# Kernel optimization log

Measured on AMD Instinct MI355X. Metric: run time of the kernel, lower is better.

The kernel has to match this reference:

```python
import jax, jax.numpy as jnp
import numpy as np

STATE_DIM = 1024
INPUT_DIM = 256
OUTPUT_DIM = 256
KX = 10
LAM = 5.0
BSZ = 16
SEQ = 2048


def setup_inputs() -> dict:
    key = jax.random.key(0)
    ks = jax.random.split(key, 6)
    inputs = jax.random.normal(ks[0], (BSZ, SEQ, INPUT_DIM), dtype=jnp.float32)
    h0 = jax.random.normal(ks[1], (STATE_DIM,), dtype=jnp.float32)
    # exponential_decay_init: entries in (exp(-lam), 1)
    A = jnp.exp(-LAM * jax.random.uniform(ks[2], (STATE_DIM,), dtype=jnp.float32))
    B = jax.random.normal(ks[3], (INPUT_DIM, STATE_DIM), dtype=jnp.float32) / INPUT_DIM
    C = jax.random.normal(ks[4], (STATE_DIM, OUTPUT_DIM), dtype=jnp.float32) / STATE_DIM
    M = jax.random.normal(ks[5], (OUTPUT_DIM, INPUT_DIM, KX), dtype=jnp.float32) / OUTPUT_DIM
    return {"inputs": inputs, "h0": h0, "A": A, "B": B, "C": C, "M": M}


def _lds_forward(inputs, h0, A, B, C, M):
    bsz, L, _ = inputs.shape
    S = A.shape[0]
    kx = M.shape[-1]
    # input projection: u_t @ B  -> [B, L, S]
    uB = jnp.einsum('bld,ds->bls', inputs, B)
    # diagonal linear recurrence h_t = A * h_{t-1} + uB_t, h_{-1} = h0,
    # via parallel associative scan on affine maps (a, b): h -> a*h + b
    a = jnp.broadcast_to(A, (1, L, S))

    def combine(x, y):
        a1, b1 = x
        a2, b2 = y
        return (a1 * a2, a2 * b1 + b2)

    Pa, Pb = jax.lax.associative_scan(combine, (a, uB), axis=1)
    all_h = Pa * h0 + Pb                              # [B, L, S]
    lds_out = jnp.einsum('bls,so->blo', all_h, C)      # [B, L, O]
    # shift forward by kx: new[:, :-kx] = lds_out[:, kx:], tail zeros
    new_lds = jnp.pad(lds_out[:, kx:, :], ((0, 0), (0, kx), (0, 0)))
    # AR term: ar[b,t,o] = sum_{i<kx} M[o,:,i] . x[b, t-i, :] (zero-padded past)
    ar = jnp.zeros_like(new_lds)
    for i in range(kx):
        x_i = jnp.pad(inputs, ((0, 0), (i, 0), (0, 0)))[:, :L, :]
        ar = ar + jnp.einsum('oj,blj->blo', M[:, :, i], x_i)
    return ar + new_lds


def reference(inputs, h0, A, B, C, M):
    return _lds_forward(inputs, h0, A, B, C, M)
```

## Files before the change

### kernel.cpp

```cpp
#include <hip/hip_runtime.h>

#define BSZn 16
#define SEQn 2048
#define DIN 256
#define DST 1024
#define DOUTn 256
#define KXn 10
#define TCH 64
#define NCH 32

typedef __attribute__((ext_vector_type(4))) float f32x4;
typedef __attribute__((ext_vector_type(8))) short bf16x8;

__device__ __forceinline__ unsigned short f2bf(float f){
  unsigned u = __float_as_uint(f);
  u += 0x7FFF + ((u>>16)&1);
  return (unsigned short)(u>>16);
}
__device__ __forceinline__ float bf2f(unsigned short s){
  return __uint_as_float(((unsigned)s)<<16);
}

#define XIDX(r,c) ((((r)<<8) + (c)) ^ (((r)&7)<<3))


__global__ void k_prep(const float* __restrict__ B, const float* __restrict__ C,
                       const float* __restrict__ M, unsigned short* __restrict__ Bt2,
                       unsigned short* __restrict__ Ct2, unsigned short* __restrict__ Mt2){
  int stride = gridDim.x*blockDim.x;
  int i0 = blockIdx.x*blockDim.x + threadIdx.x;
  for(int idx=i0; idx<DIN*DST; idx+=stride){
    int kb = idx>>15, s = (idx>>5)&1023, dl = idx&31;
    int d = (kb<<5)+dl;
    Bt2[idx] = f2bf(B[d*DST + s]);
  }
  for(int idx=i0; idx<DST*DOUTn; idx+=stride){
    int kb = idx>>13, o = (idx>>5)&255, sl = idx&31;
    int s = (kb<<5)+sl;
    Ct2[idx] = f2bf(C[s*DOUTn + o]);
  }
  for(int idx=i0; idx<DOUTn*DIN*KXn; idx+=stride){
    int kq = idx>>13, o = (idx>>5)&255, kl = idx&31;
    int k = (kq<<5)+kl, ii = k>>8, j = k&255;
    Mt2[idx] = f2bf(M[(o*DIN+j)*KXn + ii]);
  }
}

__global__ __launch_bounds__(256) void k_ub(const float* __restrict__ x,
    const unsigned short* __restrict__ Bt2, const float* __restrict__ A,
    unsigned short* __restrict__ uB, float* __restrict__ P){
  __shared__ __align__(16) unsigned short xt[64*256];
  int wg = blockIdx.x;
  int q = wg & 3, c = (wg>>2)&31, b = wg>>7;
  int t0 = c*TCH, s0 = q<<8;
  const float* xb = x + (size_t)b*SEQn*DIN;
  int tid = threadIdx.x;
  for(int e = tid; e < 64*64; e += 256){
    int r = e>>6, c4 = (e&63)<<2;
    float4 v = *(const float4*)(xb + (t0+r)*DIN + c4);
    ushort4 w; w.x=f2bf(v.x); w.y=f2bf(v.y); w.z=f2bf(v.z); w.w=f2bf(v.w);
    *(ushort4*)&xt[XIDX(r,c4)] = w;
  }
  __syncthreads();
  int wv = tid>>6, ln = tid&63, lm = ln&15, lk = (ln>>4)<<3, rr = (ln>>4)<<2;
  f32x4 zf = {0.f,0.f,0.f,0.f};
  f32x4 acc[4][4];
  #pragma unroll
  for(int tt=0;tt<4;tt++)
    #pragma unroll
    for(int nt=0;nt<4;nt++) acc[tt][nt] = zf;
  #pragma unroll
  for(int kb=0;kb<8;kb++){
    bf16x8 af[4];
    #pragma unroll
    for(int tt=0;tt<4;tt++)
      af[tt] = *(const bf16x8*)&xt[XIDX((tt<<4)+lm, (kb<<5)+lk)];
    #pragma unroll
    for(int nt=0;nt<4;nt++){
      int sg = s0 + (wv<<6) + (nt<<4) + lm;
      bf16x8 bfr = *(const bf16x8*)&Bt2[(kb<<15) + (sg<<5) + lk];
      #pragma unroll
      for(int tt=0;tt<4;tt++)
        acc[tt][nt] = __builtin_amdgcn_mfma_f32_16x16x32_bf16(af[tt], bfr, acc[tt][nt], 0,0,0);
    }
  }
  __syncthreads();
  #pragma unroll
  for(int tt=0;tt<4;tt++)
    #pragma unroll
    for(int nt=0;nt<4;nt++)
      #pragma unroll
      for(int r4=0;r4<4;r4++)
        xt[XIDX((tt<<4)+rr+r4, (wv<<6)+(nt<<4)+lm)] = f2bf(acc[tt][nt][r4]);
  __syncthreads();
  unsigned short* hb = uB + ((size_t)b*129)*32*512;
  #pragma unroll
  for(int it=0; it<8; it++){
    int j = it*256 + tid;
    int r = j>>5, c0 = (j&31)<<3;
    bf16x8 v = *(const bf16x8*)&xt[XIDX(r,c0)];
    int s = s0 + c0;
    size_t addr = (((size_t)(c*4 + (r>>4)))*32 + (s>>5))*512 + ((r&15)<<5) + (s&31);
    *(bf16x8*)&hb[addr] = v;
  }
  if(c == 31){
    unsigned* zp = (unsigned*)(uB + (((size_t)b*129 + 128)*32 + (q<<3))*512);
    for(int e = tid; e < 2048; e += 256) zp[e] = 0u;
  }
  {
    int s = s0 + tid;
    float Av = A[s];
    float p = 0.f;
    #pragma unroll
    for(int t=0;t<64;t++)
      p = fmaf(Av, p, bf2f(xt[XIDX(t, tid)]));
    P[(((b<<5)+c)<<10) + s] = p;
  }
}

__global__ void k_bound(const float* __restrict__ A, const float* __restrict__ h0,
                        const float* __restrict__ P, float* __restrict__ bound){
  int i = blockIdx.x*blockDim.x + threadIdx.x;
  if(i >= BSZn*DST) return;
  int b = i >> 10, s = i & 1023;
  float Av = A[s];
  float a2=Av*Av, a4=a2*a2, a8=a4*a4, a16=a8*a8, a32=a16*a16, a64=a32*a32;
  const float* Pb = P + ((size_t)(b<<5)<<10);
  float* Bb = bound + ((size_t)(b<<5)<<10);
  float h = h0[s];
  Bb[s] = h;
  for(int c=1;c<NCH;c++){
    h = fmaf(a64, h, Pb[((c-1)<<10)+s]);
    Bb[(c<<10)+s] = h;
  }
}

__global__ __launch_bounds__(256) void k_h(unsigned short* __restrict__ uB,
    const float* __restrict__ A, const float* __restrict__ bound){
  int wg = blockIdx.x;
  int half = wg & 1, c = (wg>>1) & 31, b = wg >> 6;
  int tid = threadIdx.x;
  int s = (half<<9) + (tid<<1);
  float Av0 = A[s], Av1 = A[s+1];
  const float* bp = bound + (((size_t)(b<<5)+c)<<10) + s;
  float h0v = bp[0], h1v = bp[1];
  unsigned short* hb = uB + (((size_t)b*129 + c*4)*32 + (s>>5))*512 + (s&31);
  #pragma unroll 4
  for(int t=0;t<64;t++){
    unsigned* p = (unsigned*)(hb + ((t>>4)*32*512) + ((t&15)<<5));
    unsigned v = *p;
    h0v = fmaf(Av0, h0v, bf2f((unsigned short)(v & 0xffff)));
    h1v = fmaf(Av1, h1v, bf2f((unsigned short)(v >> 16)));
    *p = (unsigned)f2bf(h0v) | (((unsigned)f2bf(h1v))<<16);
  }
}

__global__ __launch_bounds__(256,4) void k_arc(const float* __restrict__ x,
    const unsigned short* __restrict__ Mt2, const unsigned short* __restrict__ Ct2,
    const unsigned short* __restrict__ h2, float* __restrict__ out){
  __shared__ __align__(16) unsigned short xt[73*256];
  int wg = blockIdx.x;
  int oh = wg & 1, c = (wg>>1)&31, b = wg>>6;
  int t0 = c*TCH;
  const float* xb = x + (size_t)b*SEQn*DIN;
  int tid = threadIdx.x;
  for(int e = tid; e < 73*64; e += 256){
    int r = e>>6, c4 = (e&63)<<2;
    int t = t0 - 9 + r;
    float4 v = {0.f,0.f,0.f,0.f};
    if(t >= 0) v = *(const float4*)(xb + t*DIN + c4);
    ushort4 w; w.x=f2bf(v.x); w.y=f2bf(v.y); w.z=f2bf(v.z); w.w=f2bf(v.w);
    *(ushort4*)&xt[XIDX(r, c4)] = w;
  }
  __syncthreads();
  int wv = tid>>6, ln = tid&63, lm = ln&15, lk = (ln>>4)<<3, rr = (ln>>4)<<2;
  int obase = (oh<<7) + (wv<<5);
  f32x4 zf = {0.f,0.f,0.f,0.f};
  f32x4 acc[4][2];
  #pragma unroll
  for(int tt=0;tt<4;tt++)
    #pragma unroll
    for(int nt=0;nt<2;nt++) acc[tt][nt] = zf;
  for(int i=0;i<KXn;i++){
    #pragma unroll
    for(int kb8=0;kb8<8;kb8++){
      int col = (kb8<<5) + lk;
      int kq = i*8 + kb8;
      bf16x8 af[4];
      #pragma unroll
      for(int tt=0;tt<4;tt++)
        af[tt] = *(const bf16x8*)&xt[XIDX((tt<<4)+lm + 9 - i, col)];
      #pragma unroll
      for(int nt=0;nt<2;nt++){
        int o = obase + (nt<<4) + lm;
        bf16x8 bfr = *(const bf16x8*)&Mt2[(kq<<13) + (o<<5) + lk];
        #pragma unroll
        for(int tt=0;tt<4;tt++)
          acc[tt][nt] = __builtin_amdgcn_mfma_f32_16x16x32_bf16(af[tt], bfr, acc[tt][nt], 0,0,0);
      }
    }
  }
  const unsigned short* hb = h2 + (size_t)b*129*32*512;
  int Tg0 = c*4 + (lm>=6 ? 1 : 0);
  int rowin = (lm<6) ? (10+lm) : (lm-6);
  #pragma unroll
  for(int kb=0;kb<32;kb++){
    bf16x8 af[4];
    #pragma unroll
    for(int tt=0;tt<4;tt++)
      af[tt] = *(const bf16x8*)&hb[(((size_t)(Tg0+tt))*32 + kb)*512 + rowin*32 + lk];
    #pragma unroll
    for(int nt=0;nt<2;nt++){
      int o = obase + (nt<<4) + lm;
      bf16x8 bfr = *(const bf16x8*)&Ct2[(kb<<13) + (o<<5) + lk];
      #pragma unroll
      for(int tt=0;tt<4;tt++)
        acc[tt][nt] = __builtin_amdgcn_mfma_f32_16x16x32_bf16(af[tt], bfr, acc[tt][nt], 0,0,0);
    }
  }
  #pragma unroll
  for(int tt=0;tt<4;tt++)
    #pragma unroll
    for(int nt=0;nt<2;nt++)
      #pragma unroll
      for(int r4=0;r4<4;r4++){
        int m = (tt<<4) + rr + r4;
        int o = obase + (nt<<4) + lm;
        out[((size_t)b*SEQn + t0 + m)*DOUTn + o] = acc[tt][nt][r4];
      }
}

extern "C" void kernel_launch(void* const* d_in, const int* in_sizes, int n_in,
                              void* d_out, int out_size, void* d_ws, size_t ws_size,
                              hipStream_t stream){
  const float* x  = (const float*)d_in[0];
  const float* h0 = (const float*)d_in[1];
  const float* A  = (const float*)d_in[2];
  const float* B  = (const float*)d_in[3];
  const float* C  = (const float*)d_in[4];
  const float* M  = (const float*)d_in[5];
  float* out = (float*)d_out;
  unsigned short* Bt2 = (unsigned short*)d_ws;
  unsigned short* Ct2 = Bt2 + DIN*DST;
  unsigned short* Mt2 = Ct2 + DST*DOUTn;
  float* P     = (float*)((char*)d_ws + ( 4u<<20));
  float* bound = (float*)((char*)d_ws + ( 6u<<20));
  unsigned short* uB = (unsigned short*)((char*)d_ws + (8u<<20));
  k_prep <<<512, 256, 0, stream>>>(B, C, M, Bt2, Ct2, Mt2);
  k_ub   <<<BSZn*NCH*4, 256, 0, stream>>>(x, Bt2, A, uB, P);
  k_bound<<<(BSZn*DST)/256, 256, 0, stream>>>(A, h0, P, bound);
  k_h    <<<BSZn*NCH*2, 256, 0, stream>>>(uB, A, bound);
  k_arc  <<<BSZn*NCH*2, 256, 0, stream>>>(x, Mt2, Ct2, uB, out);
}
```

Before: 276.8 us.

## Fold chunk-boundary scan into k_h, coalesce prep reads, widen k_arc output tile

Three changes. The separate k_bound launch is removed: each k_h block now recomputes its chunk's starting state by serially folding the prior chunk sums P with A^64, which drops one launch and the bound buffer but adds up to 31 redundant reads per block. k_prep now reads the weights coalesced and scatters the bf16 writes. k_arc now has each block compute all 256 outputs (4x4 MFMA tiles per wave) with half the blocks, so each block loads the x tile once instead of twice, at the cost of more registers and less parallelism (launch bounds 256,2).

Result: faster. 255.8 us (-7.6%).

```diff
diff --git a/kernel.cpp b/kernel.cpp
--- a/kernel.cpp
+++ b/kernel.cpp
@@ -30,19 +30,18 @@
   int stride = gridDim.x*blockDim.x;
   int i0 = blockIdx.x*blockDim.x + threadIdx.x;
   for(int idx=i0; idx<DIN*DST; idx+=stride){
-    int kb = idx>>15, s = (idx>>5)&1023, dl = idx&31;
-    int d = (kb<<5)+dl;
-    Bt2[idx] = f2bf(B[d*DST + s]);
+    int d = idx>>10, s = idx&1023;
+    Bt2[((d>>5)<<15) + (s<<5) + (d&31)] = f2bf(B[idx]);
   }
   for(int idx=i0; idx<DST*DOUTn; idx+=stride){
-    int kb = idx>>13, o = (idx>>5)&255, sl = idx&31;
-    int s = (kb<<5)+sl;
-    Ct2[idx] = f2bf(C[s*DOUTn + o]);
+    int s = idx>>8, o = idx&255;
+    Ct2[((s>>5)<<13) + (o<<5) + (s&31)] = f2bf(C[idx]);
   }
   for(int idx=i0; idx<DOUTn*DIN*KXn; idx+=stride){
-    int kq = idx>>13, o = (idx>>5)&255, kl = idx&31;
-    int k = (kq<<5)+kl, ii = k>>8, j = k&255;
-    Mt2[idx] = f2bf(M[(o*DIN+j)*KXn + ii]);
+    int q = idx/KXn, ii = idx - q*KXn;
+    int o = q>>8, j = q&255;
+    int k = (ii<<8) + j;
+    Mt2[((k>>5)<<13) + (o<<5) + (k&31)] = f2bf(M[idx]);
   }
 }
 
@@ -118,49 +117,42 @@
   }
 }
 
-__global__ void k_bound(const float* __restrict__ A, const float* __restrict__ h0,
-                        const float* __restrict__ P, float* __restrict__ bound){
-  int i = blockIdx.x*blockDim.x + threadIdx.x;
-  if(i >= BSZn*DST) return;
-  int b = i >> 10, s = i & 1023;
-  float Av = A[s];
-  float a2=Av*Av, a4=a2*a2, a8=a4*a4, a16=a8*a8, a32=a16*a16, a64=a32*a32;
-  const float* Pb = P + ((size_t)(b<<5)<<10);
-  float* Bb = bound + ((size_t)(b<<5)<<10);
-  float h = h0[s];
-  Bb[s] = h;
-  for(int c=1;c<NCH;c++){
-    h = fmaf(a64, h, Pb[((c-1)<<10)+s]);
-    Bb[(c<<10)+s] = h;
-  }
-}
-
 __global__ __launch_bounds__(256) void k_h(unsigned short* __restrict__ uB,
-    const float* __restrict__ A, const float* __restrict__ bound){
+    const float* __restrict__ A, const float* __restrict__ h0,
+    const float* __restrict__ P){
   int wg = blockIdx.x;
   int half = wg & 1, c = (wg>>1) & 31, b = wg >> 6;
   int tid = threadIdx.x;
   int s = (half<<9) + (tid<<1);
-  float Av0 = A[s], Av1 = A[s+1];
-  const float* bp = bound + (((size_t)(b<<5)+c)<<10) + s;
-  float h0v = bp[0], h1v = bp[1];
+  float2 Av = *(const float2*)(A + s);
+  float a0 = Av.x, a1 = Av.y;
+  #pragma unroll
+  for(int sq=0;sq<6;sq++){ a0 *= a0; a1 *= a1; }
+  float2 hv = *(const float2*)(h0 + s);
+  float h0v = hv.x, h1v = hv.y;
+  const float2* Pb = (const float2*)(P + (((size_t)(b<<5))<<10) + s);
+  for(int j=0;j<c;j++){
+    float2 pv = Pb[(size_t)j<<9];
+    h0v = fmaf(a0, h0v, pv.x);
+    h1v = fmaf(a1, h1v, pv.y);
+  }
   unsigned short* hb = uB + (((size_t)b*129 + c*4)*32 + (s>>5))*512 + (s&31);
   #pragma unroll 4
   for(int t=0;t<64;t++){
     unsigned* p = (unsigned*)(hb + ((t>>4)*32*512) + ((t&15)<<5));
     unsigned v = *p;
-    h0v = fmaf(Av0, h0v, bf2f((unsigned short)(v & 0xffff)));
-    h1v = fmaf(Av1, h1v, bf2f((unsigned short)(v >> 16)));
+    h0v = fmaf(Av.x, h0v, bf2f((unsigned short)(v & 0xffff)));
+    h1v = fmaf(Av.y, h1v, bf2f((unsigned short)(v >> 16)));
     *p = (unsigned)f2bf(h0v) | (((unsigned)f2bf(h1v))<<16);
   }
 }
 
-__global__ __launch_bounds__(256,4) void k_arc(const float* __restrict__ x,
+__global__ __launch_bounds__(256,2) void k_arc(const float* __restrict__ x,
     const unsigned short* __restrict__ Mt2, const unsigned short* __restrict__ Ct2,
     const unsigned short* __restrict__ h2, float* __restrict__ out){
   __shared__ __align__(16) unsigned short xt[73*256];
   int wg = blockIdx.x;
-  int oh = wg & 1, c = (wg>>1)&31, b = wg>>6;
+  int b = wg>>5, c = wg&31;
   int t0 = c*TCH;
   const float* xb = x + (size_t)b*SEQn*DIN;
   int tid = threadIdx.x;
@@ -174,13 +166,13 @@
   }
   __syncthreads();
   int wv = tid>>6, ln = tid&63, lm = ln&15, lk = (ln>>4)<<3, rr = (ln>>4)<<2;
-  int obase = (oh<<7) + (wv<<5);
   f32x4 zf = {0.f,0.f,0.f,0.f};
-  f32x4 acc[4][2];
-  #pragma unroll
-  for(int tt=0;tt<4;tt++)
-    #pragma unroll
-    for(int nt=0;nt<2;nt++) acc[tt][nt] = zf;
+  f32x4 acc[4][4];
+  #pragma unroll
+  for(int tt=0;tt<4;tt++)
+    #pragma unroll
+    for(int nt=0;nt<4;nt++) acc[tt][nt] = zf;
+  #pragma unroll 2
   for(int i=0;i<KXn;i++){
     #pragma unroll
     for(int kb8=0;kb8<8;kb8++){
@@ -191,8 +183,8 @@
       for(int tt=0;tt<4;tt++)
         af[tt] = *(const bf16x8*)&xt[XIDX((tt<<4)+lm + 9 - i, col)];
       #pragma unroll
-      for(int nt=0;nt<2;nt++){
-        int o = obase + (nt<<4) + lm;
+      for(int nt=0;nt<4;nt++){
+        int o = (wv<<6) + (nt<<4) + lm;
         bf16x8 bfr = *(const bf16x8*)&Mt2[(kq<<13) + (o<<5) + lk];
         #pragma unroll
         for(int tt=0;tt<4;tt++)
@@ -210,8 +202,8 @@
     for(int tt=0;tt<4;tt++)
       af[tt] = *(const bf16x8*)&hb[(((size_t)(Tg0+tt))*32 + kb)*512 + rowin*32 + lk];
     #pragma unroll
-    for(int nt=0;nt<2;nt++){
-      int o = obase + (nt<<4) + lm;
+    for(int nt=0;nt<4;nt++){
+      int o = (wv<<6) + (nt<<4) + lm;
       bf16x8 bfr = *(const bf16x8*)&Ct2[(kb<<13) + (o<<5) + lk];
       #pragma unroll
       for(int tt=0;tt<4;tt++)
@@ -221,11 +213,11 @@
   #pragma unroll
   for(int tt=0;tt<4;tt++)
     #pragma unroll
-    for(int nt=0;nt<2;nt++)
+    for(int nt=0;nt<4;nt++)
       #pragma unroll
       for(int r4=0;r4<4;r4++){
         int m = (tt<<4) + rr + r4;
-        int o = obase + (nt<<4) + lm;
+        int o = (wv<<6) + (nt<<4) + lm;
         out[((size_t)b*SEQn + t0 + m)*DOUTn + o] = acc[tt][nt][r4];
       }
 }
@@ -244,11 +236,9 @@
   unsigned short* Ct2 = Bt2 + DIN*DST;
   unsigned short* Mt2 = Ct2 + DST*DOUTn;
   float* P     = (float*)((char*)d_ws + ( 4u<<20));
-  float* bound = (float*)((char*)d_ws + ( 6u<<20));
   unsigned short* uB = (unsigned short*)((char*)d_ws + (8u<<20));
   k_prep <<<512, 256, 0, stream>>>(B, C, M, Bt2, Ct2, Mt2);
   k_ub   <<<BSZn*NCH*4, 256, 0, stream>>>(x, Bt2, A, uB, P);
-  k_bound<<<(BSZn*DST)/256, 256, 0, stream>>>(A, h0, P, bound);
-  k_h    <<<BSZn*NCH*2, 256, 0, stream>>>(uB, A, bound);
-  k_arc  <<<BSZn*NCH*2, 256, 0, stream>>>(x, Mt2, Ct2, uB, out);
-}
+  k_h    <<<BSZn*NCH*2, 256, 0, stream>>>(uB, A, h0, P);
+  k_arc  <<<BSZn*NCH, 256, 0, stream>>>(x, Mt2, Ct2, uB, out);
+}
```
